# Optimization experiments

Measured on AMD Instinct MI355X. Metric: run time of the kernel, lower is better.

Reference implementation:

```python
import jax, jax.numpy as jnp
import numpy as np

B, S, D, H = 4, 2048, 256, 8
DH = D // H  # d_head = 32


def setup_inputs() -> dict:
    key = jax.random.key(0)
    ks = jax.random.split(key, 7)
    scale = 1.0 / np.sqrt(D)  # ~ torch Linear init range
    sequences = jax.random.normal(ks[0], (B, S, D), dtype=jnp.float32)
    Wq = jax.random.uniform(ks[1], (H, D, DH), jnp.float32, -scale, scale)
    Wk = jax.random.uniform(ks[2], (H, D, DH), jnp.float32, -scale, scale)
    Wv = jax.random.uniform(ks[3], (H, D, DH), jnp.float32, -scale, scale)
    bq = jax.random.uniform(ks[4], (H, DH), jnp.float32, -scale, scale)
    bk = jax.random.uniform(ks[5], (H, DH), jnp.float32, -scale, scale)
    bv = jax.random.uniform(ks[6], (H, DH), jnp.float32, -scale, scale)
    return {"sequences": sequences, "Wq": Wq, "Wk": Wk, "Wv": Wv,
            "bq": bq, "bk": bk, "bv": bv}


def reference(sequences, Wq, Wk, Wv, bq, bk, bv):
    # Per-head linear maps of the FULL token (use_linear_mapping=True):
    # q[b,h,s,e] = sequences[b,s,:] @ Wq[h] + bq[h]
    q = jnp.einsum('bsd,hde->bhse', sequences, Wq) + bq[None, :, None, :]
    k = jnp.einsum('bsd,hde->bhse', sequences, Wk) + bk[None, :, None, :]
    v = jnp.einsum('bsd,hde->bhse', sequences, Wv) + bv[None, :, None, :]
    # Scaled dot-product attention per batch/head (full SxS matrix, as original)
    scores = jnp.einsum('bhse,bhte->bhst', q, k) / jnp.sqrt(jnp.float32(DH))
    attn = jax.nn.softmax(scores, axis=-1)
    out = jnp.einsum('bhst,bhte->bhse', attn, v)
    # hstack heads along feature dim -> [B, S, D]
    return out.transpose(0, 2, 1, 3).reshape(B, S, D)
```

## Files before the change

kernel.cpp:

```cpp
#include <hip/hip_runtime.h>
#include <hip/hip_bf16.h>


#define NB 4
#define NS 2048
#define ND 256
#define NH 8
#define NDH 32
#define KT 128
#define NT (NS / KT)

typedef __attribute__((ext_vector_type(8))) short short8;
typedef __attribute__((ext_vector_type(4))) float float4v;
typedef __attribute__((ext_vector_type(16))) float float16v;

static __device__ __forceinline__ unsigned short f2bf(float f) {
    union { float f; unsigned int u; } v; v.f = f;
    unsigned int r = (v.u + 0x7FFFu + ((v.u >> 16) & 1u)) >> 16;
    return (unsigned short)r;
}

static __device__ __forceinline__ unsigned int pk2bf(float lo, float hi) {
    __hip_bfloat162 h = __float22bfloat162_rn(float2{lo, hi});
    union { __hip_bfloat162 h; unsigned int u; } c; c.h = h;
    return c.u;
}

#if defined(__has_builtin)
#if __has_builtin(__builtin_amdgcn_exp2f)
#define EXP2F(x) __builtin_amdgcn_exp2f(x)
#endif
#endif
#ifndef EXP2F
#define EXP2F(x) exp2f(x)
#endif

__global__ __launch_bounds__(256) void prep(const float* __restrict__ seq,
                                            unsigned short* __restrict__ seqb,
                                            const float* __restrict__ Wq,
                                            const float* __restrict__ Wk,
                                            const float* __restrict__ Wv,
                                            unsigned short* __restrict__ Wt) {
    int bx = (int)blockIdx.x;
    if (bx < 2048) {
        int i = (bx * 256 + (int)threadIdx.x) * 4;
        float4 v = *(const float4*)(seq + i);
        ushort4 o;
        o.x = f2bf(v.x); o.y = f2bf(v.y); o.z = f2bf(v.z); o.w = f2bf(v.w);
        *(ushort4*)(seqb + i) = o;
    } else {
        int idx = (bx - 2048) * 256 + (int)threadIdx.x;
        int c = idx >> 8, d = idx & 255;
        int mat = c >> 8;
        int cm = c & 255;
        int h = cm >> 5, e = cm & 31;
        const float* W = (mat == 0) ? Wq : (mat == 1) ? Wk : Wv;
        Wt[c * 256 + d] = f2bf(W[(h * 256 + d) * 32 + e]);
    }
}

__global__ __launch_bounds__(256, 2) void proj(const unsigned short* __restrict__ seqb,
                                               const unsigned short* __restrict__ Wt,
                                               const float* __restrict__ bq,
                                               const float* __restrict__ bk,
                                               const float* __restrict__ bv,
                                               unsigned short* __restrict__ Q,
                                               unsigned short* __restrict__ K,
                                               unsigned short* __restrict__ Vt) {
    __shared__ __align__(16) unsigned short plds[32768];

    int m0 = blockIdx.x * 64;
    int c0 = blockIdx.y * 64;
    int tid = (int)threadIdx.x;
    int wave = tid >> 6, lane = tid & 63;
    int g = lane >> 4, r4 = lane & 15;

#pragma unroll
    for (int j = 0; j < 16; ++j) {
        int s = tid + 256 * j;
        int local = s & 2047;
        int row = local >> 5;
        int col16 = (local & 31) ^ (row & 7);
        const unsigned short* src = (s < 2048)
            ? (seqb + (size_t)(m0 + row) * 256 + col16 * 8)
            : (Wt + (size_t)(c0 + row) * 256 + col16 * 8);
        __builtin_amdgcn_global_load_lds(
            (const __attribute__((address_space(1))) unsigned int*)src,
            (__attribute__((address_space(3))) unsigned int*)(&plds[s * 8]), 16, 0, 0);
    }
    __syncthreads();

    const unsigned short* ldsA = plds;
    const unsigned short* ldsB = plds + 16384;
    int rowA = wave * 16 + r4;
    int xA = r4 & 7;

    float4v acc[4];
#pragma unroll
    for (int ct = 0; ct < 4; ++ct) acc[ct] = (float4v){0.f, 0.f, 0.f, 0.f};

#pragma unroll
    for (int i = 0; i < 8; ++i) {
        int cp = ((4 * i + g) ^ xA) * 8;
        short8 a = *(const short8*)(ldsA + rowA * 256 + cp);
#pragma unroll
        for (int ct = 0; ct < 4; ++ct) {
            short8 b = *(const short8*)(ldsB + (ct * 16 + r4) * 256 + cp);
            acc[ct] = __builtin_amdgcn_mfma_f32_16x16x32_bf16(a, b, acc[ct], 0, 0, 0);
        }
    }

    const float SC = 0.17677669529663687f * 1.4426950408889634f;
#pragma unroll
    for (int ct = 0; ct < 4; ++ct) {
        int c = c0 + ct * 16 + r4;
        int mat = c >> 8;
        int cm = c & 255;
        int h = cm >> 5, e = cm & 31;
        float bias = ((mat == 0) ? bq : (mat == 1) ? bk : bv)[cm];
#pragma unroll
        for (int r = 0; r < 4; ++r) {
            int m = m0 + wave * 16 + 4 * g + r;
            int b = m >> 11, s = m & 2047;
            float val = acc[ct][r] + bias;
            if (mat == 0) {
                Q[((b * NH + h) * NS + s) * NDH + e] = f2bf(val * SC);
            } else if (mat == 1) {
                K[((b * NH + h) * NS + s) * NDH + e] = f2bf(val);
            } else {
                Vt[((b * NH + h) * NDH + e) * NS + s] = f2bf(val);
            }
        }
    }
}

__global__ __launch_bounds__(256, 2) void attn_kernel(const unsigned short* __restrict__ Q,
                                                      const unsigned short* __restrict__ K,
                                                      const unsigned short* __restrict__ Vt,
                                                      float* __restrict__ out) {
    __shared__ __align__(16) unsigned short lds[3][8192];

    int bx = (int)blockIdx.x;
    int wid = (bx & 7) * 64 + (bx >> 3);
    int bh = wid >> 4;
    int qt = wid & 15;
    int tid = (int)threadIdx.x;
    int wave = tid >> 6, lane = tid & 63;
    int r31 = lane & 31, hi2 = lane >> 5;
    int q0 = qt * 128 + wave * 32;

    const unsigned short* Qb = Q + (size_t)bh * NS * NDH;
    const unsigned short* Kb = K + (size_t)bh * NS * NDH;
    const unsigned short* Vb = Vt + (size_t)bh * NDH * NS;

    const unsigned short* sgp;
    int strideT;
    int strideB;
    unsigned int sloff;
    {
        int s = tid & 127;
        int row = s >> 2;
        int srcC = (s & 3) ^ ((row >> 1) & 3);
        if (tid < 128) {
            int key = (row & ~12) | ((row & 4) << 1) | ((row & 8) >> 1);
            sgp = Kb + key * NDH + srcC * 8;
            strideT = KT * NDH;
            strideB = 32 * NDH;
            sloff = s * 8;
        } else {
            sgp = Vb + row * NS + srcC * 8;
            strideT = KT;
            strideB = 32;
            sloff = 1024 + s * 8;
        }
    }

#define STAGE(bufi, t)                                                                        \
    do {                                                                                      \
        const unsigned short* _s = sgp + (size_t)(t) * strideT;                               \
        __builtin_amdgcn_global_load_lds(                                                     \
            (const __attribute__((address_space(1))) unsigned int*)(_s),                      \
            (__attribute__((address_space(3))) unsigned int*)(&lds[bufi][sloff]), 16, 0, 0);  \
        __builtin_amdgcn_global_load_lds(                                                     \
            (const __attribute__((address_space(1))) unsigned int*)(_s + strideB),            \
            (__attribute__((address_space(3))) unsigned int*)(&lds[bufi][sloff + 2048]), 16, 0, 0); \
        __builtin_amdgcn_global_load_lds(                                                     \
            (const __attribute__((address_space(1))) unsigned int*)(_s + 2 * strideB),        \
            (__attribute__((address_space(3))) unsigned int*)(&lds[bufi][sloff + 4096]), 16, 0, 0); \
        __builtin_amdgcn_global_load_lds(                                                     \
            (const __attribute__((address_space(1))) unsigned int*)(_s + 3 * strideB),        \
            (__attribute__((address_space(3))) unsigned int*)(&lds[bufi][sloff + 6144]), 16, 0, 0); \
    } while (0)

    int rx = (r31 >> 1) & 3;
    int kOffA = r31 * 64 + ((hi2 ^ rx) << 4);
    int kOffB = r31 * 64 + (((2 + hi2) ^ rx) << 4);
    int vOffA = 2048 + r31 * 64 + ((hi2 ^ rx) << 4);
    int vOffB = 2048 + r31 * 64 + (((2 + hi2) ^ rx) << 4);

    const unsigned short* qrow = Qb + (q0 + r31) * NDH;
    short8 qa = *(const short8*)(qrow + 8 * hi2);
    short8 qb = *(const short8*)(qrow + 16 + 8 * hi2);

    float16v accE = {0.f}, accO = {0.f};
    const float16v zero16 = {0.f};
    float lp = 0.f;

    auto process = [&](const char* buf, float16v& acc) {
        short8 kfA = *(const short8*)(buf + kOffA);
        short8 kfB = *(const short8*)(buf + kOffB);
        short8 vfA = *(const short8*)(buf + vOffA);
        short8 vfB = *(const short8*)(buf + vOffB);
        float16v s = __builtin_amdgcn_mfma_f32_32x32x16_bf16(kfA, qa, zero16, 0, 0, 0);
        s = __builtin_amdgcn_mfma_f32_32x32x16_bf16(kfB, qb, s, 0, 0, 0);
        float p[16];
#pragma unroll
        for (int r = 0; r < 16; ++r) p[r] = EXP2F(s[r]);
#pragma unroll
        for (int r = 0; r < 16; ++r) lp += p[r];
        union { short8 v; unsigned int u[4]; } pb1, pb2;
#pragma unroll
        for (int w = 0; w < 4; ++w) {
            pb1.u[w] = pk2bf(p[2 * w], p[2 * w + 1]);
            pb2.u[w] = pk2bf(p[8 + 2 * w], p[9 + 2 * w]);
        }
        acc = __builtin_amdgcn_mfma_f32_32x32x16_bf16(vfA, pb1.v, acc, 0, 0, 0);
        acc = __builtin_amdgcn_mfma_f32_32x32x16_bf16(vfB, pb2.v, acc, 0, 0, 0);
    };

    STAGE(0, 0);
    STAGE(1, 1);

    int cur = 0;
    for (int t = 0; t < NT; ++t) {
        __builtin_amdgcn_s_barrier();
        if (t + 2 < NT) {
            int fut = cur + 2; if (fut >= 3) fut -= 3;
            STAGE(fut, t + 2);
            asm volatile("s_waitcnt vmcnt(8)" ::: "memory");
        } else if (t + 1 < NT) {
            asm volatile("s_waitcnt vmcnt(4)" ::: "memory");
        } else {
            asm volatile("s_waitcnt vmcnt(0)" ::: "memory");
        }
        __builtin_amdgcn_sched_barrier(0);

        __builtin_amdgcn_s_setprio(1);
        const char* buf = (const char*)lds[cur];
        process(buf, accE);
        process(buf + 4096, accO);
        process(buf + 8192, accE);
        process(buf + 12288, accO);
        __builtin_amdgcn_s_setprio(0);

        __builtin_amdgcn_sched_barrier(0);
        ++cur; if (cur >= 3) cur -= 3;
    }

    lp += __shfl_xor(lp, 32);
    float linv = 1.0f / lp;
    float16v accT = accE + accO;

    int b = bh >> 3, h = bh & 7;
    int srow = q0 + r31;
    float* op = out + (size_t)(b * NS + srow) * ND + h * NDH + 4 * hi2;
#pragma unroll
    for (int i = 0; i < 4; ++i) {
        float4 o4 = {accT[4 * i] * linv, accT[4 * i + 1] * linv,
                     accT[4 * i + 2] * linv, accT[4 * i + 3] * linv};
        *(float4*)(op + 8 * i) = o4;
    }
#undef STAGE
}

extern "C" void kernel_launch(void* const* d_in, const int* in_sizes, int n_in,
                              void* d_out, int out_size, void* d_ws, size_t ws_size,
                              hipStream_t stream) {
    const float* seq = (const float*)d_in[0];
    const float* Wq = (const float*)d_in[1];
    const float* Wk = (const float*)d_in[2];
    const float* Wv = (const float*)d_in[3];
    const float* bq = (const float*)d_in[4];
    const float* bk = (const float*)d_in[5];
    const float* bv = (const float*)d_in[6];
    float* out = (float*)d_out;

    unsigned short* seqb = (unsigned short*)d_ws;
    unsigned short* Wt = seqb + 2097152;
    unsigned short* Qw = Wt + 196608;
    unsigned short* Kw = Qw + 2097152;
    unsigned short* Vtw = Kw + 2097152;

    hipLaunchKernelGGL(prep, dim3(2816), dim3(256), 0, stream, seq, seqb, Wq, Wk, Wv, Wt);
    hipLaunchKernelGGL(proj, dim3(128, 12), dim3(256), 0, stream, seqb, Wt, bq, bk, bv, Qw, Kw, Vtw);
    hipLaunchKernelGGL(attn_kernel, dim3(512), dim3(256), 0, stream, Qw, Kw, Vtw, out);
}
```

Baseline: 58.23 us.

## Split attention KV range across waves with per-wave staging and LDS reduction

The attention kernel now gives each block 64 queries, and each of its four waves handles a quarter of the keys. Each wave stages K/V into its own double buffer, which removes block-wide barriers from the main loop. The per-wave partial outputs and row sums are then combined through LDS at the end. The grid doubles to 1024 blocks and the launch bound asks for 4 blocks per CU, trading more work per wave and a final reduction for better occupancy and no inter-wave synchronization.

```diff
diff --git a/kernel.cpp b/kernel.cpp
--- a/kernel.cpp
+++ b/kernel.cpp
@@ -7,8 +7,8 @@
 #define ND 256
 #define NH 8
 #define NDH 32
-#define KT 128
-#define NT (NS / KT)
+#define KW 512
+#define NTW (KW / 32)
 
 typedef __attribute__((ext_vector_type(8))) short short8;
 typedef __attribute__((ext_vector_type(4))) float float4v;
@@ -134,62 +134,56 @@
     }
 }
 
-__global__ __launch_bounds__(256, 2) void attn_kernel(const unsigned short* __restrict__ Q,
+__global__ __launch_bounds__(256, 4) void attn_kernel(const unsigned short* __restrict__ Q,
                                                       const unsigned short* __restrict__ K,
                                                       const unsigned short* __restrict__ Vt,
                                                       float* __restrict__ out) {
-    __shared__ __align__(16) unsigned short lds[3][8192];
+    __shared__ __align__(16) char smem[37888];
 
     int bx = (int)blockIdx.x;
-    int wid = (bx & 7) * 64 + (bx >> 3);
-    int bh = wid >> 4;
-    int qt = wid & 15;
+    int wid = (bx & 7) * 128 + (bx >> 3);
+    int bh = wid >> 5;
+    int qt = wid & 31;
     int tid = (int)threadIdx.x;
     int wave = tid >> 6, lane = tid & 63;
     int r31 = lane & 31, hi2 = lane >> 5;
-    int q0 = qt * 128 + wave * 32;
+    int q0 = qt * 64;
+    int kv0 = wave * KW;
 
     const unsigned short* Qb = Q + (size_t)bh * NS * NDH;
     const unsigned short* Kb = K + (size_t)bh * NS * NDH;
     const unsigned short* Vb = Vt + (size_t)bh * NDH * NS;
 
-    const unsigned short* sgp;
-    int strideT;
-    int strideB;
-    unsigned int sloff;
-    {
-        int s = tid & 127;
-        int row = s >> 2;
-        int srcC = (s & 3) ^ ((row >> 1) & 3);
-        if (tid < 128) {
-            int key = (row & ~12) | ((row & 4) << 1) | ((row & 8) >> 1);
-            sgp = Kb + key * NDH + srcC * 8;
-            strideT = KT * NDH;
-            strideB = 32 * NDH;
-            sloff = s * 8;
-        } else {
-            sgp = Vb + row * NS + srcC * 8;
-            strideT = KT;
-            strideB = 32;
-            sloff = 1024 + s * 8;
-        }
-    }
-
-#define STAGE(bufi, t)                                                                        \
-    do {                                                                                      \
-        const unsigned short* _s = sgp + (size_t)(t) * strideT;                               \
-        __builtin_amdgcn_global_load_lds(                                                     \
-            (const __attribute__((address_space(1))) unsigned int*)(_s),                      \
-            (__attribute__((address_space(3))) unsigned int*)(&lds[bufi][sloff]), 16, 0, 0);  \
-        __builtin_amdgcn_global_load_lds(                                                     \
-            (const __attribute__((address_space(1))) unsigned int*)(_s + strideB),            \
-            (__attribute__((address_space(3))) unsigned int*)(&lds[bufi][sloff + 2048]), 16, 0, 0); \
-        __builtin_amdgcn_global_load_lds(                                                     \
-            (const __attribute__((address_space(1))) unsigned int*)(_s + 2 * strideB),        \
-            (__attribute__((address_space(3))) unsigned int*)(&lds[bufi][sloff + 4096]), 16, 0, 0); \
-        __builtin_amdgcn_global_load_lds(                                                     \
-            (const __attribute__((address_space(1))) unsigned int*)(_s + 3 * strideB),        \
-            (__attribute__((address_space(3))) unsigned int*)(&lds[bufi][sloff + 6144]), 16, 0, 0); \
+    auto mkK = [&](int slot) -> const unsigned short* {
+        int row = slot >> 2;
+        int srcC = (slot & 3) ^ ((row >> 1) & 3);
+        int key = (row & ~12) | ((row & 4) << 1) | ((row & 8) >> 1);
+        return Kb + (size_t)(kv0 + key) * NDH + srcC * 8;
+    };
+    auto mkV = [&](int sp) -> const unsigned short* {
+        int row = sp >> 2;
+        int srcC = (sp & 3) ^ ((row >> 1) & 3);
+        return Vb + (size_t)row * NS + kv0 + srcC * 8;
+    };
+    const unsigned short* sp0 = mkK(lane);
+    const unsigned short* sp1 = mkK(64 + lane);
+    const unsigned short* sp2 = mkV(lane);
+    const unsigned short* sp3 = mkV(64 + lane);
+
+    char* bufA = smem + wave * 8192;
+    char* bufB = bufA + 4096;
+
+#define GLD(srcp, dstp)                                                        \
+    __builtin_amdgcn_global_load_lds(                                          \
+        (const __attribute__((address_space(1))) unsigned int*)(srcp),         \
+        (__attribute__((address_space(3))) unsigned int*)(dstp), 16, 0, 0)
+
+#define STAGE(bufp, t)                                                         \
+    do {                                                                       \
+        GLD(sp0 + (t) * 1024, (bufp) + lane * 16);                             \
+        GLD(sp1 + (t) * 1024, (bufp) + 1024 + lane * 16);                      \
+        GLD(sp2 + (t) * 32,   (bufp) + 2048 + lane * 16);                      \
+        GLD(sp3 + (t) * 32,   (bufp) + 3072 + lane * 16);                      \
     } while (0)
 
     int rx = (r31 >> 1) & 3;
@@ -198,79 +192,127 @@
     int vOffA = 2048 + r31 * 64 + ((hi2 ^ rx) << 4);
     int vOffB = 2048 + r31 * 64 + (((2 + hi2) ^ rx) << 4);
 
-    const unsigned short* qrow = Qb + (q0 + r31) * NDH;
-    short8 qa = *(const short8*)(qrow + 8 * hi2);
-    short8 qb = *(const short8*)(qrow + 16 + 8 * hi2);
-
-    float16v accE = {0.f}, accO = {0.f};
+    const unsigned short* qrow0 = Qb + (q0 + r31) * NDH;
+    const unsigned short* qrow1 = Qb + (q0 + 32 + r31) * NDH;
+    short8 qa0 = *(const short8*)(qrow0 + 8 * hi2);
+    short8 qb0 = *(const short8*)(qrow0 + 16 + 8 * hi2);
+    short8 qa1 = *(const short8*)(qrow1 + 8 * hi2);
+    short8 qb1 = *(const short8*)(qrow1 + 16 + 8 * hi2);
+    asm volatile("s_waitcnt vmcnt(0)" ::: "memory");
+    __builtin_amdgcn_sched_barrier(0);
+
+    float16v acc0 = {0.f}, acc1 = {0.f};
     const float16v zero16 = {0.f};
-    float lp = 0.f;
-
-    auto process = [&](const char* buf, float16v& acc) {
+    float l0 = 0.f, l1 = 0.f;
+
+    auto process = [&](const char* buf) {
         short8 kfA = *(const short8*)(buf + kOffA);
         short8 kfB = *(const short8*)(buf + kOffB);
         short8 vfA = *(const short8*)(buf + vOffA);
         short8 vfB = *(const short8*)(buf + vOffB);
-        float16v s = __builtin_amdgcn_mfma_f32_32x32x16_bf16(kfA, qa, zero16, 0, 0, 0);
-        s = __builtin_amdgcn_mfma_f32_32x32x16_bf16(kfB, qb, s, 0, 0, 0);
-        float p[16];
-#pragma unroll
-        for (int r = 0; r < 16; ++r) p[r] = EXP2F(s[r]);
-#pragma unroll
-        for (int r = 0; r < 16; ++r) lp += p[r];
-        union { short8 v; unsigned int u[4]; } pb1, pb2;
-#pragma unroll
-        for (int w = 0; w < 4; ++w) {
-            pb1.u[w] = pk2bf(p[2 * w], p[2 * w + 1]);
-            pb2.u[w] = pk2bf(p[8 + 2 * w], p[9 + 2 * w]);
-        }
-        acc = __builtin_amdgcn_mfma_f32_32x32x16_bf16(vfA, pb1.v, acc, 0, 0, 0);
-        acc = __builtin_amdgcn_mfma_f32_32x32x16_bf16(vfB, pb2.v, acc, 0, 0, 0);
+        {
+            float16v s = __builtin_amdgcn_mfma_f32_32x32x16_bf16(kfA, qa0, zero16, 0, 0, 0);
+            s = __builtin_amdgcn_mfma_f32_32x32x16_bf16(kfB, qb0, s, 0, 0, 0);
+            float p[16];
+#pragma unroll
+            for (int r = 0; r < 16; ++r) p[r] = EXP2F(s[r]);
+#pragma unroll
+            for (int r = 0; r < 16; ++r) l0 += p[r];
+            union { short8 v; unsigned int u[4]; } pb1, pb2;
+#pragma unroll
+            for (int w = 0; w < 4; ++w) {
+                pb1.u[w] = pk2bf(p[2 * w], p[2 * w + 1]);
+                pb2.u[w] = pk2bf(p[8 + 2 * w], p[9 + 2 * w]);
+            }
+            acc0 = __builtin_amdgcn_mfma_f32_32x32x16_bf16(vfA, pb1.v, acc0, 0, 0, 0);
+            acc0 = __builtin_amdgcn_mfma_f32_32x32x16_bf16(vfB, pb2.v, acc0, 0, 0, 0);
+        }
+        {
+            float16v s = __builtin_amdgcn_mfma_f32_32x32x16_bf16(kfA, qa1, zero16, 0, 0, 0);
+            s = __builtin_amdgcn_mfma_f32_32x32x16_bf16(kfB, qb1, s, 0, 0, 0);
+            float p[16];
+#pragma unroll
+            for (int r = 0; r < 16; ++r) p[r] = EXP2F(s[r]);
+#pragma unroll
+            for (int r = 0; r < 16; ++r) l1 += p[r];
+            union { short8 v; unsigned int u[4]; } pb1, pb2;
+#pragma unroll
+            for (int w = 0; w < 4; ++w) {
+                pb1.u[w] = pk2bf(p[2 * w], p[2 * w + 1]);
+                pb2.u[w] = pk2bf(p[8 + 2 * w], p[9 + 2 * w]);
+            }
+            acc1 = __builtin_amdgcn_mfma_f32_32x32x16_bf16(vfA, pb1.v, acc1, 0, 0, 0);
+            acc1 = __builtin_amdgcn_mfma_f32_32x32x16_bf16(vfB, pb2.v, acc1, 0, 0, 0);
+        }
     };
 
-    STAGE(0, 0);
-    STAGE(1, 1);
-
-    int cur = 0;
-    for (int t = 0; t < NT; ++t) {
-        __builtin_amdgcn_s_barrier();
-        if (t + 2 < NT) {
-            int fut = cur + 2; if (fut >= 3) fut -= 3;
-            STAGE(fut, t + 2);
-            asm volatile("s_waitcnt vmcnt(8)" ::: "memory");
-        } else if (t + 1 < NT) {
+    STAGE(bufA, 0);
+    for (int t = 0; t < NTW; t += 2) {
+        STAGE(bufB, t + 1);
+        asm volatile("s_waitcnt vmcnt(4)" ::: "memory");
+        __builtin_amdgcn_sched_barrier(0);
+        __builtin_amdgcn_s_setprio(1);
+        process(bufA);
+        __builtin_amdgcn_s_setprio(0);
+
+        if (t + 2 < NTW) {
+            STAGE(bufA, t + 2);
             asm volatile("s_waitcnt vmcnt(4)" ::: "memory");
         } else {
             asm volatile("s_waitcnt vmcnt(0)" ::: "memory");
         }
         __builtin_amdgcn_sched_barrier(0);
-
         __builtin_amdgcn_s_setprio(1);
-        const char* buf = (const char*)lds[cur];
-        process(buf, accE);
-        process(buf + 4096, accO);
-        process(buf + 8192, accE);
-        process(buf + 12288, accO);
+        process(bufB);
         __builtin_amdgcn_s_setprio(0);
-
-        __builtin_amdgcn_sched_barrier(0);
-        ++cur; if (cur >= 3) cur -= 3;
-    }
-
-    lp += __shfl_xor(lp, 32);
-    float linv = 1.0f / lp;
-    float16v accT = accE + accO;
-
-    int b = bh >> 3, h = bh & 7;
-    int srow = q0 + r31;
-    float* op = out + (size_t)(b * NS + srow) * ND + h * NDH + 4 * hi2;
-#pragma unroll
-    for (int i = 0; i < 4; ++i) {
-        float4 o4 = {accT[4 * i] * linv, accT[4 * i + 1] * linv,
-                     accT[4 * i + 2] * linv, accT[4 * i + 3] * linv};
-        *(float4*)(op + 8 * i) = o4;
+    }
+
+    l0 += __shfl_xor(l0, 32);
+    l1 += __shfl_xor(l1, 32);
+
+    __syncthreads();
+    float* part = (float*)smem;
+    float* pll = (float*)(smem + 36864);
+#pragma unroll
+    for (int j = 0; j < 2; ++j) {
+        int qlocal = 32 * j + r31;
+        float* prow = part + (wave * 64 + qlocal) * 36 + 4 * hi2;
+        const float16v& A = j ? acc1 : acc0;
+#pragma unroll
+        for (int i = 0; i < 4; ++i) {
+            float4 v4 = {A[4 * i], A[4 * i + 1], A[4 * i + 2], A[4 * i + 3]};
+            *(float4*)(prow + 8 * i) = v4;
+        }
+    }
+    if (lane < 32) {
+        pll[wave * 64 + r31] = l0;
+        pll[wave * 64 + 32 + r31] = l1;
+    }
+    __syncthreads();
+
+    {
+        int q = tid >> 2, ch = tid & 3;
+        float lsum = pll[q] + pll[64 + q] + pll[128 + q] + pll[192 + q];
+        float inv = 1.0f / lsum;
+        float4 s0 = {0.f, 0.f, 0.f, 0.f}, s1 = {0.f, 0.f, 0.f, 0.f};
+#pragma unroll
+        for (int w = 0; w < 4; ++w) {
+            const float* prow = part + (w * 64 + q) * 36 + ch * 8;
+            float4 a = *(const float4*)(prow);
+            float4 b = *(const float4*)(prow + 4);
+            s0.x += a.x; s0.y += a.y; s0.z += a.z; s0.w += a.w;
+            s1.x += b.x; s1.y += b.y; s1.z += b.z; s1.w += b.w;
+        }
+        s0.x *= inv; s0.y *= inv; s0.z *= inv; s0.w *= inv;
+        s1.x *= inv; s1.y *= inv; s1.z *= inv; s1.w *= inv;
+        int b = bh >> 3, h = bh & 7;
+        int srow = q0 + q;
+        float* op = out + (size_t)(b * NS + srow) * ND + h * NDH + ch * 8;
+        *(float4*)(op) = s0;
+        *(float4*)(op + 4) = s1;
     }
 #undef STAGE
+#undef GLD
 }
 
 extern "C" void kernel_launch(void* const* d_in, const int* in_sizes, int n_in,
@@ -293,5 +335,5 @@
 
     hipLaunchKernelGGL(prep, dim3(2816), dim3(256), 0, stream, seq, seqb, Wq, Wk, Wv, Wt);
     hipLaunchKernelGGL(proj, dim3(128, 12), dim3(256), 0, stream, seqb, Wt, bq, bk, bv, Qw, Kw, Vtw);
-    hipLaunchKernelGGL(attn_kernel, dim3(512), dim3(256), 0, stream, Qw, Kw, Vtw, out);
-}
+    hipLaunchKernelGGL(attn_kernel, dim3(1024), dim3(256), 0, stream, Qw, Kw, Vtw, out);
+}
```

After: 58.31 us. About the same (+0.1%).
